# Performance work log

Measured on AMD Instinct MI355X. Metric: run time of the kernel, lower is better.

Reference implementation:

```python
import jax, jax.numpy as jnp
import numpy as np

B, S, D, H, DFF = 2, 2048, 2048, 16, 8192
DH = D // H
EPS = 1e-5


def _layer_norm(x, g, b):
    mu = jnp.mean(x, axis=-1, keepdims=True)
    var = jnp.mean(jnp.square(x - mu), axis=-1, keepdims=True)
    return (x - mu) * jax.lax.rsqrt(var + EPS) * g + b


def setup_inputs() -> dict:
    key = jax.random.key(0)
    ks = jax.random.split(key, 12)
    sc = 0.02
    inp = {
        "x": jax.random.normal(ks[0], (B, S, D), dtype=jnp.float32),
        # attention projections, stored [in, out] (torch Linear weight transposed)
        "wq": jax.random.normal(ks[1], (D, D), dtype=jnp.float32) * sc,
        "bq": jnp.zeros((D,), jnp.float32),
        "wk": jax.random.normal(ks[2], (D, D), dtype=jnp.float32) * sc,
        "bk": jnp.zeros((D,), jnp.float32),
        "wv": jax.random.normal(ks[3], (D, D), dtype=jnp.float32) * sc,
        "bv": jnp.zeros((D,), jnp.float32),
        "wo": jax.random.normal(ks[4], (D, D), dtype=jnp.float32) * sc,
        "bo": jnp.zeros((D,), jnp.float32),
        "ln1_g": jnp.ones((D,), jnp.float32),
        "ln1_b": jnp.zeros((D,), jnp.float32),
        # feed-forward
        "w1": jax.random.normal(ks[5], (D, DFF), dtype=jnp.float32) * sc,
        "b1": jnp.zeros((DFF,), jnp.float32),
        "w2": jax.random.normal(ks[6], (DFF, D), dtype=jnp.float32) * sc,
        "b2": jnp.zeros((D,), jnp.float32),
        "ln2_g": jnp.ones((D,), jnp.float32),
        "ln2_b": jnp.zeros((D,), jnp.float32),
    }
    return inp


def reference(x, wq, bq, wk, bk, wv, bv, wo, bo, ln1_g, ln1_b,
              w1, b1, w2, b2, ln2_g, ln2_b):
    # ---- MultiHeadAttentionBlock: x + MHA(LN(x)) ----
    h = _layer_norm(x, ln1_g, ln1_b)                      # [B,S,D]
    q = (h @ wq + bq).reshape(B, S, H, DH).transpose(0, 2, 1, 3)  # [B,H,S,DH]
    k = (h @ wk + bk).reshape(B, S, H, DH).transpose(0, 2, 1, 3)
    v = (h @ wv + bv).reshape(B, S, H, DH).transpose(0, 2, 1, 3)

    # faithful to source: scale by sqrt(d_dim), NOT sqrt(head_dim)
    scores = jnp.einsum("bhqd,bhkd->bhqk", q, k) / np.sqrt(D).astype(np.float32)
    # faithful triu/transpose masking (softmax sees raw zeros, not -inf)
    t = jnp.triu(scores).swapaxes(-2, -1)                 # [B,H,S,S]
    s = jax.nn.softmax(t, axis=-2)
    r = jnp.triu(s).swapaxes(-2, -1)
    attn = jnp.einsum("bhqk,bhkd->bhqd", r, v)            # [B,H,S,DH]
    attn = attn.transpose(0, 2, 1, 3).reshape(B, S, D)
    x = x + attn @ wo + bo

    # ---- FeedForwardBlock: x + FF(LN(x)), dropout rate 0 ----
    h2 = _layer_norm(x, ln2_g, ln2_b)
    ff = jax.nn.relu(h2 @ w1 + b1) @ w2 + b2
    return x + ff
```

## Files before the change

kernel.cpp:

```cpp
#include <hip/hip_runtime.h>


typedef unsigned short ushort_t;
typedef unsigned int   uint32;
typedef __attribute__((ext_vector_type(8))) short    short8;
typedef __attribute__((ext_vector_type(8))) ushort_t ushort8;
typedef __attribute__((ext_vector_type(4))) float    f32x4;

#define BDIM   2
#define SEQ    2048
#define DMODEL 2048
#define NHEAD  16
#define DHEAD  128
#define DFFN   8192
#define MROWS  (BDIM*SEQ)
#define LDQKV  6144

#define GPTR(p) (const __attribute__((address_space(1))) void*)((const void*)(p))
#define SPTR(p) (__attribute__((address_space(3))) void*)((void*)(p))

__device__ __forceinline__ float bf2f(ushort_t u) {
  union { uint32 i; float f; } c; c.i = ((uint32)u) << 16; return c.f;
}
__device__ __forceinline__ ushort_t f2bf(float f) {
  union { float f; uint32 i; } c; c.f = f;
  uint32 u = c.i;
  return (ushort_t)((u + 0x7fffu + ((u >> 16) & 1u)) >> 16);
}

__global__ __launch_bounds__(256) void transpose_f32_bf16_kern(
    const float* __restrict__ W, ushort_t* __restrict__ Wt, int K, int N)
{
  __shared__ float tile[32][33];
  const int nb = blockIdx.x * 32, kb = blockIdx.y * 32;
  const int tx = threadIdx.x & 31, ty = threadIdx.x >> 5;
#pragma unroll
  for (int j = 0; j < 32; j += 8)
    tile[ty + j][tx] = W[(size_t)(kb + ty + j) * N + nb + tx];
  __syncthreads();
#pragma unroll
  for (int j = 0; j < 32; j += 8)
    Wt[(size_t)(nb + ty + j) * K + kb + tx] = f2bf(tile[tx][ty + j]);
}

__global__ __launch_bounds__(256) void bias_concat_kern(
    const float* __restrict__ a, const float* __restrict__ b,
    const float* __restrict__ c, float* __restrict__ o)
{
  const int i = blockIdx.x * 256 + threadIdx.x;
  o[i] = (i < 2048) ? a[i] : ((i < 4096) ? b[i - 2048] : c[i - 4096]);
}

__global__ __launch_bounds__(256) void ln_kern(
    const float* __restrict__ X, const float* __restrict__ G,
    const float* __restrict__ Bb, ushort_t* __restrict__ Out)
{
  const int row = blockIdx.x, tid = threadIdx.x;
  const float* xr = X + (size_t)row * DMODEL;
  float4 v0 = ((const float4*)xr)[tid * 2];
  float4 v1 = ((const float4*)xr)[tid * 2 + 1];
  float s  = v0.x + v0.y + v0.z + v0.w + v1.x + v1.y + v1.z + v1.w;
  float ss = v0.x*v0.x + v0.y*v0.y + v0.z*v0.z + v0.w*v0.w
           + v1.x*v1.x + v1.y*v1.y + v1.z*v1.z + v1.w*v1.w;
#pragma unroll
  for (int off = 32; off > 0; off >>= 1) {
    s  += __shfl_down(s, off);
    ss += __shfl_down(ss, off);
  }
  __shared__ float rs[4], rss[4];
  __shared__ float sh_mu, sh_rst;
  const int wv = tid >> 6;
  if ((tid & 63) == 0) { rs[wv] = s; rss[wv] = ss; }
  __syncthreads();
  if (tid == 0) {
    float S1 = rs[0] + rs[1] + rs[2] + rs[3];
    float S2 = rss[0] + rss[1] + rss[2] + rss[3];
    float mu = S1 * (1.f / DMODEL);
    float var = S2 * (1.f / DMODEL) - mu * mu;
    sh_mu = mu;
    sh_rst = rsqrtf(var + 1e-5f);
  }
  __syncthreads();
  const float mu = sh_mu, rst = sh_rst;
  float4 g0 = ((const float4*)G)[tid * 2];
  float4 g1 = ((const float4*)G)[tid * 2 + 1];
  float4 b0 = ((const float4*)Bb)[tid * 2];
  float4 b1 = ((const float4*)Bb)[tid * 2 + 1];
  ushort8 o;
  o[0] = f2bf((v0.x - mu) * rst * g0.x + b0.x);
  o[1] = f2bf((v0.y - mu) * rst * g0.y + b0.y);
  o[2] = f2bf((v0.z - mu) * rst * g0.z + b0.z);
  o[3] = f2bf((v0.w - mu) * rst * g0.w + b0.w);
  o[4] = f2bf((v1.x - mu) * rst * g1.x + b1.x);
  o[5] = f2bf((v1.y - mu) * rst * g1.y + b1.y);
  o[6] = f2bf((v1.z - mu) * rst * g1.z + b1.z);
  o[7] = f2bf((v1.w - mu) * rst * g1.w + b1.w);
  *(ushort8*)(Out + (size_t)row * DMODEL + tid * 8) = o;
}

template<int OUT, int RELU, int RESID, int KDIV>
__global__ __launch_bounds__(512, 2) void gemm8_kern(
    const ushort_t* __restrict__ A, const ushort_t* __restrict__ Bt,
    const float* __restrict__ bias, const float* __restrict__ resid,
    void* __restrict__ Cout, int M, int N, int K)
{
  __shared__ ushort_t sA[4 * 8192];
  __shared__ ushort_t sB[4 * 8192];

  const int tid = threadIdx.x;
  const int nM  = gridDim.y;
  const int nwg = gridDim.x * nM;
  const int bid = blockIdx.y * gridDim.x + blockIdx.x;
  const int cpx = nwg >> 3;
  const int swz = (bid & 7) * cpx + (bid >> 3);
  const int m0 = (swz % nM) * 256;
  const int n0 = (swz / nM) * 256;

  const int Keff = K / KDIV;
  const int k0 = (KDIV > 1) ? blockIdx.z * Keff : 0;
  const int T = Keff >> 6;

  const int l = tid & 63, w = tid >> 6;
  const int lr = l & 15, lg = l >> 4;
  const int wr = w >> 2, wc = w & 3;

  const int xch   = (lg ^ ((lr >> 1) & 3)) * 8;
  const int abase = (wr * 128 + lr) * 32 + xch;
  const int bbase = (wc * 64  + lr) * 32 + xch;

  const int sr = tid >> 2;
  const int sg = ((tid & 3) ^ ((tid >> 3) & 3)) * 8;
  const ushort_t* Asrc = A  + (size_t)(m0 + sr) * K + k0 + sg;
  const ushort_t* Bsrc = Bt + (size_t)(n0 + sr) * K + k0 + sg;
  ushort_t* dA = sA + tid * 8;
  ushort_t* dB = sB + tid * 8;

#define SA_(slot, kt, kk, r) __builtin_amdgcn_global_load_lds( \
    GPTR(Asrc + (size_t)(r) * 128 * K + (kt) * 64 + (kk) * 32), \
    SPTR(dA + (slot) * 8192 + (r) * 4096), 16, 0, 0)
#define SB_(slot, kt, kk, r) __builtin_amdgcn_global_load_lds( \
    GPTR(Bsrc + (size_t)(r) * 128 * K + (kt) * 64 + (kk) * 32), \
    SPTR(dB + (slot) * 8192 + (r) * 4096), 16, 0, 0)

  f32x4 acc[8][4] = {};

  SA_(0, 0, 0, 0); SA_(0, 0, 0, 1); SB_(0, 0, 0, 0); SB_(0, 0, 0, 1);
  SA_(1, 0, 1, 0); SA_(1, 0, 1, 1); SB_(1, 0, 1, 0); SB_(1, 0, 1, 1);
  SA_(2, 1, 0, 0); SA_(2, 1, 0, 1); SB_(2, 1, 0, 0); SB_(2, 1, 0, 1);
  asm volatile("s_waitcnt vmcnt(8)" ::: "memory");
  __builtin_amdgcn_s_barrier();

  for (int t = 0; t < T; ++t) {
    const int c = t & 1;
    const ushort_t* A0 = sA + (c * 2 + 0) * 8192;
    const ushort_t* B0 = sB + (c * 2 + 0) * 8192;
    const ushort_t* A1 = sA + (c * 2 + 1) * 8192;
    const ushort_t* B1 = sB + (c * 2 + 1) * 8192;
    const int s1 = (c ^ 1) * 2 + 1;
    const int s0 = c * 2;
    const bool pf1 = (t + 1 < T), pf0 = (t + 2 < T);

    short8 a0, a1, a2, a3, b0, b1, b2, b3;

    b0 = *(const short8*)(B0 + bbase);
    b1 = *(const short8*)(B0 + bbase + 512);
    b2 = *(const short8*)(B0 + bbase + 1024);
    b3 = *(const short8*)(B0 + bbase + 1536);
    a0 = *(const short8*)(A0 + abase);
    a1 = *(const short8*)(A0 + abase + 512);
    a2 = *(const short8*)(A0 + abase + 1024);
    a3 = *(const short8*)(A0 + abase + 1536);
    if (pf1) { SA_(s1, t + 1, 1, 0); SA_(s1, t + 1, 1, 1); }
    __builtin_amdgcn_s_setprio(1);
    acc[0][0] = __builtin_amdgcn_mfma_f32_16x16x32_bf16(a0, b0, acc[0][0], 0, 0, 0);
    acc[0][1] = __builtin_amdgcn_mfma_f32_16x16x32_bf16(a0, b1, acc[0][1], 0, 0, 0);
    acc[0][2] = __builtin_amdgcn_mfma_f32_16x16x32_bf16(a0, b2, acc[0][2], 0, 0, 0);
    acc[0][3] = __builtin_amdgcn_mfma_f32_16x16x32_bf16(a0, b3, acc[0][3], 0, 0, 0);
    acc[1][0] = __builtin_amdgcn_mfma_f32_16x16x32_bf16(a1, b0, acc[1][0], 0, 0, 0);
    acc[1][1] = __builtin_amdgcn_mfma_f32_16x16x32_bf16(a1, b1, acc[1][1], 0, 0, 0);
    acc[1][2] = __builtin_amdgcn_mfma_f32_16x16x32_bf16(a1, b2, acc[1][2], 0, 0, 0);
    acc[1][3] = __builtin_amdgcn_mfma_f32_16x16x32_bf16(a1, b3, acc[1][3], 0, 0, 0);
    acc[2][0] = __builtin_amdgcn_mfma_f32_16x16x32_bf16(a2, b0, acc[2][0], 0, 0, 0);
    acc[2][1] = __builtin_amdgcn_mfma_f32_16x16x32_bf16(a2, b1, acc[2][1], 0, 0, 0);
    acc[2][2] = __builtin_amdgcn_mfma_f32_16x16x32_bf16(a2, b2, acc[2][2], 0, 0, 0);
    acc[2][3] = __builtin_amdgcn_mfma_f32_16x16x32_bf16(a2, b3, acc[2][3], 0, 0, 0);
    acc[3][0] = __builtin_amdgcn_mfma_f32_16x16x32_bf16(a3, b0, acc[3][0], 0, 0, 0);
    acc[3][1] = __builtin_amdgcn_mfma_f32_16x16x32_bf16(a3, b1, acc[3][1], 0, 0, 0);
    acc[3][2] = __builtin_amdgcn_mfma_f32_16x16x32_bf16(a3, b2, acc[3][2], 0, 0, 0);
    acc[3][3] = __builtin_amdgcn_mfma_f32_16x16x32_bf16(a3, b3, acc[3][3], 0, 0, 0);
    __builtin_amdgcn_s_setprio(0);

    a0 = *(const short8*)(A0 + abase + 2048);
    a1 = *(const short8*)(A0 + abase + 2560);
    a2 = *(const short8*)(A0 + abase + 3072);
    a3 = *(const short8*)(A0 + abase + 3584);
    if (pf1) { SB_(s1, t + 1, 1, 0); SB_(s1, t + 1, 1, 1); }
    __builtin_amdgcn_s_setprio(1);
    acc[4][0] = __builtin_amdgcn_mfma_f32_16x16x32_bf16(a0, b0, acc[4][0], 0, 0, 0);
    acc[4][1] = __builtin_amdgcn_mfma_f32_16x16x32_bf16(a0, b1, acc[4][1], 0, 0, 0);
    acc[4][2] = __builtin_amdgcn_mfma_f32_16x16x32_bf16(a0, b2, acc[4][2], 0, 0, 0);
    acc[4][3] = __builtin_amdgcn_mfma_f32_16x16x32_bf16(a0, b3, acc[4][3], 0, 0, 0);
    acc[5][0] = __builtin_amdgcn_mfma_f32_16x16x32_bf16(a1, b0, acc[5][0], 0, 0, 0);
    acc[5][1] = __builtin_amdgcn_mfma_f32_16x16x32_bf16(a1, b1, acc[5][1], 0, 0, 0);
    acc[5][2] = __builtin_amdgcn_mfma_f32_16x16x32_bf16(a1, b2, acc[5][2], 0, 0, 0);
    acc[5][3] = __builtin_amdgcn_mfma_f32_16x16x32_bf16(a1, b3, acc[5][3], 0, 0, 0);
    acc[6][0] = __builtin_amdgcn_mfma_f32_16x16x32_bf16(a2, b0, acc[6][0], 0, 0, 0);
    acc[6][1] = __builtin_amdgcn_mfma_f32_16x16x32_bf16(a2, b1, acc[6][1], 0, 0, 0);
    acc[6][2] = __builtin_amdgcn_mfma_f32_16x16x32_bf16(a2, b2, acc[6][2], 0, 0, 0);
    acc[6][3] = __builtin_amdgcn_mfma_f32_16x16x32_bf16(a2, b3, acc[6][3], 0, 0, 0);
    acc[7][0] = __builtin_amdgcn_mfma_f32_16x16x32_bf16(a3, b0, acc[7][0], 0, 0, 0);
    acc[7][1] = __builtin_amdgcn_mfma_f32_16x16x32_bf16(a3, b1, acc[7][1], 0, 0, 0);
    acc[7][2] = __builtin_amdgcn_mfma_f32_16x16x32_bf16(a3, b2, acc[7][2], 0, 0, 0);
    acc[7][3] = __builtin_amdgcn_mfma_f32_16x16x32_bf16(a3, b3, acc[7][3], 0, 0, 0);
    __builtin_amdgcn_s_setprio(0);
    if (t < T - 2) { asm volatile("s_waitcnt vmcnt(8)" ::: "memory"); }
    else           { asm volatile("s_waitcnt vmcnt(0)" ::: "memory"); }
    __builtin_amdgcn_s_barrier();

    b0 = *(const short8*)(B1 + bbase);
    b1 = *(const short8*)(B1 + bbase + 512);
    b2 = *(const short8*)(B1 + bbase + 1024);
    b3 = *(const short8*)(B1 + bbase + 1536);
    a0 = *(const short8*)(A1 + abase);
    a1 = *(const short8*)(A1 + abase + 512);
    a2 = *(const short8*)(A1 + abase + 1024);
    a3 = *(const short8*)(A1 + abase + 1536);
    if (pf0) { SA_(s0, t + 2, 0, 0); SA_(s0, t + 2, 0, 1); }
    __builtin_amdgcn_s_setprio(1);
    acc[0][0] = __builtin_amdgcn_mfma_f32_16x16x32_bf16(a0, b0, acc[0][0], 0, 0, 0);
    acc[0][1] = __builtin_amdgcn_mfma_f32_16x16x32_bf16(a0, b1, acc[0][1], 0, 0, 0);
    acc[0][2] = __builtin_amdgcn_mfma_f32_16x16x32_bf16(a0, b2, acc[0][2], 0, 0, 0);
    acc[0][3] = __builtin_amdgcn_mfma_f32_16x16x32_bf16(a0, b3, acc[0][3], 0, 0, 0);
    acc[1][0] = __builtin_amdgcn_mfma_f32_16x16x32_bf16(a1, b0, acc[1][0], 0, 0, 0);
    acc[1][1] = __builtin_amdgcn_mfma_f32_16x16x32_bf16(a1, b1, acc[1][1], 0, 0, 0);
    acc[1][2] = __builtin_amdgcn_mfma_f32_16x16x32_bf16(a1, b2, acc[1][2], 0, 0, 0);
    acc[1][3] = __builtin_amdgcn_mfma_f32_16x16x32_bf16(a1, b3, acc[1][3], 0, 0, 0);
    acc[2][0] = __builtin_amdgcn_mfma_f32_16x16x32_bf16(a2, b0, acc[2][0], 0, 0, 0);
    acc[2][1] = __builtin_amdgcn_mfma_f32_16x16x32_bf16(a2, b1, acc[2][1], 0, 0, 0);
    acc[2][2] = __builtin_amdgcn_mfma_f32_16x16x32_bf16(a2, b2, acc[2][2], 0, 0, 0);
    acc[2][3] = __builtin_amdgcn_mfma_f32_16x16x32_bf16(a2, b3, acc[2][3], 0, 0, 0);
    acc[3][0] = __builtin_amdgcn_mfma_f32_16x16x32_bf16(a3, b0, acc[3][0], 0, 0, 0);
    acc[3][1] = __builtin_amdgcn_mfma_f32_16x16x32_bf16(a3, b1, acc[3][1], 0, 0, 0);
    acc[3][2] = __builtin_amdgcn_mfma_f32_16x16x32_bf16(a3, b2, acc[3][2], 0, 0, 0);
    acc[3][3] = __builtin_amdgcn_mfma_f32_16x16x32_bf16(a3, b3, acc[3][3], 0, 0, 0);
    __builtin_amdgcn_s_setprio(0);

    a0 = *(const short8*)(A1 + abase + 2048);
    a1 = *(const short8*)(A1 + abase + 2560);
    a2 = *(const short8*)(A1 + abase + 3072);
    a3 = *(const short8*)(A1 + abase + 3584);
    if (pf0) { SB_(s0, t + 2, 0, 0); SB_(s0, t + 2, 0, 1); }
    __builtin_amdgcn_s_setprio(1);
    acc[4][0] = __builtin_amdgcn_mfma_f32_16x16x32_bf16(a0, b0, acc[4][0], 0, 0, 0);
    acc[4][1] = __builtin_amdgcn_mfma_f32_16x16x32_bf16(a0, b1, acc[4][1], 0, 0, 0);
    acc[4][2] = __builtin_amdgcn_mfma_f32_16x16x32_bf16(a0, b2, acc[4][2], 0, 0, 0);
    acc[4][3] = __builtin_amdgcn_mfma_f32_16x16x32_bf16(a0, b3, acc[4][3], 0, 0, 0);
    acc[5][0] = __builtin_amdgcn_mfma_f32_16x16x32_bf16(a1, b0, acc[5][0], 0, 0, 0);
    acc[5][1] = __builtin_amdgcn_mfma_f32_16x16x32_bf16(a1, b1, acc[5][1], 0, 0, 0);
    acc[5][2] = __builtin_amdgcn_mfma_f32_16x16x32_bf16(a1, b2, acc[5][2], 0, 0, 0);
    acc[5][3] = __builtin_amdgcn_mfma_f32_16x16x32_bf16(a1, b3, acc[5][3], 0, 0, 0);
    acc[6][0] = __builtin_amdgcn_mfma_f32_16x16x32_bf16(a2, b0, acc[6][0], 0, 0, 0);
    acc[6][1] = __builtin_amdgcn_mfma_f32_16x16x32_bf16(a2, b1, acc[6][1], 0, 0, 0);
    acc[6][2] = __builtin_amdgcn_mfma_f32_16x16x32_bf16(a2, b2, acc[6][2], 0, 0, 0);
    acc[6][3] = __builtin_amdgcn_mfma_f32_16x16x32_bf16(a2, b3, acc[6][3], 0, 0, 0);
    acc[7][0] = __builtin_amdgcn_mfma_f32_16x16x32_bf16(a3, b0, acc[7][0], 0, 0, 0);
    acc[7][1] = __builtin_amdgcn_mfma_f32_16x16x32_bf16(a3, b1, acc[7][1], 0, 0, 0);
    acc[7][2] = __builtin_amdgcn_mfma_f32_16x16x32_bf16(a3, b2, acc[7][2], 0, 0, 0);
    acc[7][3] = __builtin_amdgcn_mfma_f32_16x16x32_bf16(a3, b3, acc[7][3], 0, 0, 0);
    __builtin_amdgcn_s_setprio(0);
    if (t < T - 2) { asm volatile("s_waitcnt vmcnt(8)" ::: "memory"); }
    else           { asm volatile("s_waitcnt vmcnt(0)" ::: "memory"); }
    __builtin_amdgcn_s_barrier();
  }
#undef SA_
#undef SB_

  ushort_t* Pz = (OUT == 2)
      ? (ushort_t*)Cout + (size_t)blockIdx.z * M * N : (ushort_t*)Cout;
#pragma unroll
  for (int mi = 0; mi < 8; ++mi) {
#pragma unroll
    for (int ni = 0; ni < 4; ++ni) {
      const int gn = n0 + wc * 64 + ni * 16 + lr;
      const float bvv = (OUT == 2) ? 0.f : bias[gn];
#pragma unroll
      for (int j = 0; j < 4; ++j) {
        const int gm = m0 + wr * 128 + mi * 16 + lg * 4 + j;
        float v = acc[mi][ni][j] + bvv;
        if (RESID) v += resid[(size_t)gm * N + gn];
        if (RELU) v = fmaxf(v, 0.f);
        if (OUT == 0)      ((float*)Cout)[(size_t)gm * N + gn] = v;
        else               Pz[(size_t)gm * N + gn] = f2bf(v);
      }
    }
  }
}

__global__ __launch_bounds__(256) void combine_kern(
    const ushort_t* __restrict__ pp, const float* __restrict__ bias,
    const float* __restrict__ resid, float* __restrict__ out)
{
  const size_t i = ((size_t)blockIdx.x * 256 + threadIdx.x) * 8;
  ushort8 p0 = *(const ushort8*)(pp + i);
  ushort8 p1 = *(const ushort8*)(pp + (size_t)MROWS * 2048 + i);
  const int col = (int)(i & 2047);
  float4 r0 = *(const float4*)(resid + i);
  float4 r1 = *(const float4*)(resid + i + 4);
  float4 c0 = *(const float4*)(bias + col);
  float4 c1 = *(const float4*)(bias + col + 4);
  float4 o0, o1;
  o0.x = bf2f(p0[0]) + bf2f(p1[0]) + c0.x + r0.x;
  o0.y = bf2f(p0[1]) + bf2f(p1[1]) + c0.y + r0.y;
  o0.z = bf2f(p0[2]) + bf2f(p1[2]) + c0.z + r0.z;
  o0.w = bf2f(p0[3]) + bf2f(p1[3]) + c0.w + r0.w;
  o1.x = bf2f(p0[4]) + bf2f(p1[4]) + c1.x + r1.x;
  o1.y = bf2f(p0[5]) + bf2f(p1[5]) + c1.y + r1.y;
  o1.z = bf2f(p0[6]) + bf2f(p1[6]) + c1.z + r1.z;
  o1.w = bf2f(p0[7]) + bf2f(p1[7]) + c1.w + r1.w;
  *(float4*)(out + i) = o0;
  *(float4*)(out + i + 4) = o1;
}

__global__ __launch_bounds__(256) void attn_stats_kern(
    const ushort_t* __restrict__ Q, const ushort_t* __restrict__ Kb,
    float* __restrict__ E, float* __restrict__ DG, int ld)
{
  __shared__ ushort_t Ksm[64 * 128];
  const int qb = blockIdx.x;
  const int bh = blockIdx.y;
  const int b = bh >> 4, h = bh & 15;
  const int tid = threadIdx.x;
  const int l = tid & 63, w = tid >> 6;
  const int lr = l & 15, lg = l >> 4;

  const int qrow0 = qb * 64 + w * 16;

  const size_t qoff = (size_t)(b * SEQ + qrow0 + lr) * ld + h * DHEAD + lg * 8;
  short8 af[4];
#pragma unroll
  for (int c = 0; c < 4; ++c) af[c] = *(const short8*)(Q + qoff + c * 32);

  const int srow_b = w * 16 + (l >> 4);
  const ushort_t* Kg = Kb + (size_t)b * SEQ * ld + (size_t)h * DHEAD;
  ushort_t* Sbase = Ksm + w * 2048;

  f32x4 sume = {0.f, 0.f, 0.f, 0.f};
  f32x4 dge  = {0.f, 0.f, 0.f, 0.f};
  const float scale = 0.0220970869120796f;
  const int rx = lr & 7;

  for (int kc = qb; kc < 32; ++kc) {
    __syncthreads();
#pragma unroll
    for (int c = 0; c < 4; ++c) {
      const int row = srow_b + c * 4;
      const int g = (l & 15) ^ (row & 7);
      __builtin_amdgcn_global_load_lds(
          GPTR(Kg + (size_t)(kc * 64 + row) * ld + g * 8),
          SPTR(Sbase + c * 512), 16, 0, 0);
    }
    __syncthreads();

    const int ks0 = (kc == qb) ? w : 0;
    for (int ks = ks0; ks < 4; ++ks) {
      short8 bfr[4];
#pragma unroll
      for (int c = 0; c < 4; ++c)
        bfr[c] = *(const short8*)(Ksm + (ks * 16 + lr) * 128 + ((lg + c * 4) ^ rx) * 8);
      f32x4 sc = {0.f, 0.f, 0.f, 0.f};
      sc = __builtin_amdgcn_mfma_f32_16x16x32_bf16(af[0], bfr[0], sc, 0, 0, 0);
      sc = __builtin_amdgcn_mfma_f32_16x16x32_bf16(af[1], bfr[1], sc, 0, 0, 0);
      sc = __builtin_amdgcn_mfma_f32_16x16x32_bf16(af[2], bfr[2], sc, 0, 0, 0);
      sc = __builtin_amdgcn_mfma_f32_16x16x32_bf16(af[3], bfr[3], sc, 0, 0, 0);
      if (kc == qb && ks == w) {
        const int ki = kc * 64 + ks * 16 + lr;
#pragma unroll
        for (int j = 0; j < 4; ++j) {
          const int qi = qrow0 + lg * 4 + j;
          if (ki >= qi) {
            float e = __expf(sc[j] * scale);
            sume[j] += e;
            if (ki == qi) dge[j] += e;
          }
        }
      } else {
#pragma unroll
        for (int j = 0; j < 4; ++j)
          sume[j] += __expf(sc[j] * scale);
      }
    }
  }

#pragma unroll
  for (int j = 0; j < 4; ++j) {
#pragma unroll
    for (int off = 1; off < 16; off <<= 1) {
      sume[j] += __shfl_xor(sume[j], off);
      dge[j]  += __shfl_xor(dge[j], off);
    }
  }
  if (lr == 0) {
#pragma unroll
    for (int j = 0; j < 4; ++j) {
      E[(size_t)bh * SEQ + qrow0 + lg * 4 + j]  = sume[j];
      DG[(size_t)bh * SEQ + qrow0 + lg * 4 + j] = dge[j];
    }
  }
}

__global__ __launch_bounds__(128) void vchunk_kern(
    const ushort_t* __restrict__ V, float* __restrict__ CS, int ld)
{
  const int c = blockIdx.x, bh = blockIdx.y;
  const int b = bh >> 4, h = bh & 15;
  const int dh = threadIdx.x;
  const ushort_t* vp = V + (size_t)(b * SEQ + c * 64) * ld + h * DHEAD + dh;
  float s = 0.f;
  for (int i = 0; i < 64; ++i) s += bf2f(vp[(size_t)i * ld]);
  CS[((size_t)bh * 32 + c) * 128 + dh] = s;
}

__global__ __launch_bounds__(128) void attn_combine_kern(
    const ushort_t* __restrict__ V, const float* __restrict__ CS,
    const float* __restrict__ E, const float* __restrict__ DG,
    ushort_t* __restrict__ Attn, int ldv)
{
  const int c = blockIdx.x, bh = blockIdx.y;
  const int b = bh >> 4, h = bh & 15;
  const int dh = threadIdx.x;
  float prefix = 0.f;
  for (int cc = 0; cc < c; ++cc) prefix += CS[((size_t)bh * 32 + cc) * 128 + dh];
  const ushort_t* vp = V + (size_t)(b * SEQ + c * 64) * ldv + h * DHEAD + dh;
  ushort_t* ap = Attn + (size_t)(b * SEQ + c * 64) * DMODEL + h * DHEAD + dh;
  const int qb = c * 64;
  for (int i = 0; i < 64; ++i) {
    const int qq = qb + i;
    const float denom = (float)qq + E[(size_t)bh * SEQ + qq];
    const float de = DG[(size_t)bh * SEQ + qq];
    const float vv = bf2f(vp[(size_t)i * ldv]);
    ap[(size_t)i * DMODEL] = f2bf((prefix + de * vv) / denom);
    prefix += vv;
  }
}

extern "C" void kernel_launch(void* const* d_in, const int* in_sizes, int n_in,
                              void* d_out, int out_size, void* d_ws, size_t ws_size,
                              hipStream_t stream)
{
  const float* x    = (const float*)d_in[0];
  const float* wq   = (const float*)d_in[1];
  const float* bq   = (const float*)d_in[2];
  const float* wk   = (const float*)d_in[3];
  const float* bk   = (const float*)d_in[4];
  const float* wv   = (const float*)d_in[5];
  const float* bv   = (const float*)d_in[6];
  const float* wo   = (const float*)d_in[7];
  const float* bo   = (const float*)d_in[8];
  const float* ln1g = (const float*)d_in[9];
  const float* ln1b = (const float*)d_in[10];
  const float* w1   = (const float*)d_in[11];
  const float* b1   = (const float*)d_in[12];
  const float* w2   = (const float*)d_in[13];
  const float* b2   = (const float*)d_in[14];
  const float* ln2g = (const float*)d_in[15];
  const float* ln2b = (const float*)d_in[16];
  float* out = (float*)d_out;

  char* ws = (char*)d_ws;
  ushort_t* W1T  = (ushort_t*)(ws + 0);
  ushort_t* PPf2 = (ushort_t*)(ws + 0);
  ushort_t* W2T  = (ushort_t*)(ws + 33554432);
  ushort_t* WOT  = (ushort_t*)(ws + 67108864);
  float*    X2   = (float*)   (ws + 75497472);
  float*    Bcat = (float*)   (ws + 75497472);
  ushort_t* Hb   = (ushort_t*)(ws + 109051904);
  ushort_t* F1   = (ushort_t*)(ws + 125829120);
  ushort_t* PPwo = (ushort_t*)(ws + 125829120);
  ushort_t* WQKV = (ushort_t*)(ws + 125829120);
  ushort_t* QKVb = (ushort_t*)(ws + 150994944);
  float*    Eb   = (float*)   (ws + 201326592);
  float*    DGb  = (float*)   (ws + 201588736);
  float*    CSb  = (float*)   (ws + 201850880);

  transpose_f32_bf16_kern<<<dim3(64, 64),  256, 0, stream>>>(wq, WQKV,                   2048, 2048);
  transpose_f32_bf16_kern<<<dim3(64, 64),  256, 0, stream>>>(wk, WQKV + 2048 * 2048,     2048, 2048);
  transpose_f32_bf16_kern<<<dim3(64, 64),  256, 0, stream>>>(wv, WQKV + 2 * 2048 * 2048, 2048, 2048);
  transpose_f32_bf16_kern<<<dim3(64, 64),  256, 0, stream>>>(wo, WOT, 2048, 2048);
  transpose_f32_bf16_kern<<<dim3(256, 64), 256, 0, stream>>>(w1, W1T, 2048, 8192);
  transpose_f32_bf16_kern<<<dim3(64, 256), 256, 0, stream>>>(w2, W2T, 8192, 2048);
  bias_concat_kern<<<24, 256, 0, stream>>>(bq, bk, bv, Bcat);

  ln_kern<<<MROWS, 256, 0, stream>>>(x, ln1g, ln1b, Hb);

  gemm8_kern<1, 0, 0, 1><<<dim3(24, 16), 512, 0, stream>>>(
      Hb, WQKV, Bcat, nullptr, QKVb, MROWS, LDQKV, DMODEL);

  attn_stats_kern<<<dim3(32, 32), 256, 0, stream>>>(QKVb, QKVb + 2048, Eb, DGb, LDQKV);

  vchunk_kern<<<dim3(32, 32), 128, 0, stream>>>(QKVb + 4096, CSb, LDQKV);
  attn_combine_kern<<<dim3(32, 32), 128, 0, stream>>>(QKVb + 4096, CSb, Eb, DGb, Hb, LDQKV);

  gemm8_kern<2, 0, 0, 2><<<dim3(8, 16, 2), 512, 0, stream>>>(
      Hb, WOT, bo, nullptr, PPwo, MROWS, DMODEL, DMODEL);
  combine_kern<<<4096, 256, 0, stream>>>(PPwo, bo, x, X2);

  ln_kern<<<MROWS, 256, 0, stream>>>(X2, ln2g, ln2b, Hb);

  gemm8_kern<1, 1, 0, 1><<<dim3(32, 16), 512, 0, stream>>>(
      Hb, W1T, b1, nullptr, F1, MROWS, DFFN, DMODEL);

  gemm8_kern<2, 0, 0, 2><<<dim3(8, 16, 2), 512, 0, stream>>>(
      F1, W2T, b2, nullptr, PPf2, MROWS, DMODEL, DFFN);
  combine_kern<<<4096, 256, 0, stream>>>(PPf2, b2, X2, out);
}
```

Measured before the change: 654.2 us.

## Switch GEMMs to 32x32 MFMA, fuse weight prep and combine+LayerNorm

The GEMM kernel now uses 32x32x16 bf16 MFMA instructions with a 4x2 accumulator tile per wave instead of 16x16x32 with 8x4. This is meant to cut LDS fragment reads and instruction count per flop. Separately, the six weight transposes and the bias concat are merged into a single launch. The residual combine is fused with the second LayerNorm, removing a kernel and a pass over the activations. Risks are a changed LDS access pattern that could cause bank conflicts, and different register pressure under the 512x2 launch bounds.

```diff
diff --git a/kernel.cpp b/kernel.cpp
--- a/kernel.cpp
+++ b/kernel.cpp
@@ -3,9 +3,10 @@
 
 typedef unsigned short ushort_t;
 typedef unsigned int   uint32;
-typedef __attribute__((ext_vector_type(8))) short    short8;
-typedef __attribute__((ext_vector_type(8))) ushort_t ushort8;
-typedef __attribute__((ext_vector_type(4))) float    f32x4;
+typedef __attribute__((ext_vector_type(8)))  short    short8;
+typedef __attribute__((ext_vector_type(8)))  ushort_t ushort8;
+typedef __attribute__((ext_vector_type(4)))  float    f32x4;
+typedef __attribute__((ext_vector_type(16))) float    f32x16;
 
 #define BDIM   2
 #define SEQ    2048
@@ -28,11 +29,34 @@
   return (ushort_t)((u + 0x7fffu + ((u >> 16) & 1u)) >> 16);
 }
 
-__global__ __launch_bounds__(256) void transpose_f32_bf16_kern(
-    const float* __restrict__ W, ushort_t* __restrict__ Wt, int K, int N)
-{
+__global__ __launch_bounds__(256) void prep_kern(
+    const float* __restrict__ wq, const float* __restrict__ wk,
+    const float* __restrict__ wv, const float* __restrict__ wo,
+    const float* __restrict__ w1, const float* __restrict__ w2,
+    const float* __restrict__ bq, const float* __restrict__ bk,
+    const float* __restrict__ bv,
+    ushort_t* __restrict__ WQKV, ushort_t* __restrict__ WOT,
+    ushort_t* __restrict__ W1T, ushort_t* __restrict__ W2T,
+    float* __restrict__ Bcat)
+{
+  const int bid = blockIdx.x;
+  if (bid >= 49152) {
+    for (int i = threadIdx.x; i < 6144; i += 256)
+      Bcat[i] = (i < 2048) ? bq[i] : ((i < 4096) ? bk[i - 2048] : bv[i - 4096]);
+    return;
+  }
+  const float* W; ushort_t* Wt; int K, N, local;
+  if (bid < 12288) {
+    const int which = bid >> 12; local = bid & 4095;
+    W = (which == 0) ? wq : (which == 1) ? wk : wv;
+    Wt = WQKV + (size_t)which * 2048 * 2048; K = 2048; N = 2048;
+  } else if (bid < 16384) { W = wo; Wt = WOT; K = 2048; N = 2048; local = bid - 12288; }
+  else if (bid < 32768)   { W = w1; Wt = W1T; K = 2048; N = 8192; local = bid - 16384; }
+  else                    { W = w2; Wt = W2T; K = 8192; N = 2048; local = bid - 32768; }
+  const int ntiles = N >> 5;
+  const int nb = (local % ntiles) * 32, kb = (local / ntiles) * 32;
+
   __shared__ float tile[32][33];
-  const int nb = blockIdx.x * 32, kb = blockIdx.y * 32;
   const int tx = threadIdx.x & 31, ty = threadIdx.x >> 5;
 #pragma unroll
   for (int j = 0; j < 32; j += 8)
@@ -41,14 +65,6 @@
 #pragma unroll
   for (int j = 0; j < 32; j += 8)
     Wt[(size_t)(nb + ty + j) * K + kb + tx] = f2bf(tile[tx][ty + j]);
-}
-
-__global__ __launch_bounds__(256) void bias_concat_kern(
-    const float* __restrict__ a, const float* __restrict__ b,
-    const float* __restrict__ c, float* __restrict__ o)
-{
-  const int i = blockIdx.x * 256 + threadIdx.x;
-  o[i] = (i < 2048) ? a[i] : ((i < 4096) ? b[i - 2048] : c[i - 4096]);
 }
 
 __global__ __launch_bounds__(256) void ln_kern(
@@ -98,11 +114,58 @@
   *(ushort8*)(Out + (size_t)row * DMODEL + tid * 8) = o;
 }
 
-template<int OUT, int RELU, int RESID, int KDIV>
-__global__ __launch_bounds__(512, 2) void gemm8_kern(
+__global__ __launch_bounds__(256) void combine_ln_kern(
+    const ushort_t* __restrict__ pp, const float* __restrict__ bias,
+    const float* __restrict__ xres, const float* __restrict__ G,
+    const float* __restrict__ Bb, float* __restrict__ X2,
+    ushort_t* __restrict__ Out)
+{
+  const int row = blockIdx.x, tid = threadIdx.x;
+  const size_t i = (size_t)row * DMODEL + tid * 8;
+  ushort8 p0 = *(const ushort8*)(pp + i);
+  ushort8 p1 = *(const ushort8*)(pp + (size_t)MROWS * 2048 + i);
+  float v[8];
+#pragma unroll
+  for (int j = 0; j < 8; ++j)
+    v[j] = bf2f(p0[j]) + bf2f(p1[j]) + bias[tid * 8 + j] + xres[i + j];
+  float4 o0 = {v[0], v[1], v[2], v[3]}, o1 = {v[4], v[5], v[6], v[7]};
+  *(float4*)(X2 + i) = o0;
+  *(float4*)(X2 + i + 4) = o1;
+
+  float s = 0.f, ss = 0.f;
+#pragma unroll
+  for (int j = 0; j < 8; ++j) { s += v[j]; ss += v[j] * v[j]; }
+#pragma unroll
+  for (int off = 32; off > 0; off >>= 1) {
+    s  += __shfl_down(s, off);
+    ss += __shfl_down(ss, off);
+  }
+  __shared__ float rs[4], rss[4];
+  __shared__ float sh_mu, sh_rst;
+  const int wvv = tid >> 6;
+  if ((tid & 63) == 0) { rs[wvv] = s; rss[wvv] = ss; }
+  __syncthreads();
+  if (tid == 0) {
+    float S1 = rs[0] + rs[1] + rs[2] + rs[3];
+    float S2 = rss[0] + rss[1] + rss[2] + rss[3];
+    float mu = S1 * (1.f / DMODEL);
+    float var = S2 * (1.f / DMODEL) - mu * mu;
+    sh_mu = mu; sh_rst = rsqrtf(var + 1e-5f);
+  }
+  __syncthreads();
+  const float mu = sh_mu, rst = sh_rst;
+  ushort8 o;
+#pragma unroll
+  for (int j = 0; j < 8; ++j)
+    o[j] = f2bf((v[j] - mu) * rst * G[tid * 8 + j] + Bb[tid * 8 + j]);
+  *(ushort8*)(Out + i) = o;
+}
+
+template<int OUT, int RELU, int KDIV>
+__global__ __launch_bounds__(512, 2) void gemm32_kern(
     const ushort_t* __restrict__ A, const ushort_t* __restrict__ Bt,
-    const float* __restrict__ bias, const float* __restrict__ resid,
-    void* __restrict__ Cout, int M, int N, int K)
+    const float* __restrict__ bias, void* __restrict__ Cout,
+    int M, int N, int K)
 {
   __shared__ ushort_t sA[4 * 8192];
   __shared__ ushort_t sB[4 * 8192];
@@ -121,12 +184,14 @@
   const int T = Keff >> 6;
 
   const int l = tid & 63, w = tid >> 6;
-  const int lr = l & 15, lg = l >> 4;
+  const int l31 = l & 31, kh = l >> 5;
   const int wr = w >> 2, wc = w & 3;
 
-  const int xch   = (lg ^ ((lr >> 1) & 3)) * 8;
-  const int abase = (wr * 128 + lr) * 32 + xch;
-  const int bbase = (wc * 64  + lr) * 32 + xch;
+  const int rx2 = (l31 >> 1) & 3;
+  const int xo0 = ((0 + kh) ^ rx2) * 8;
+  const int xo1 = ((2 + kh) ^ rx2) * 8;
+  const int arow = (wr * 128 + l31) * 32;
+  const int brow = (wc * 64  + l31) * 32;
 
   const int sr = tid >> 2;
   const int sg = ((tid & 3) ^ ((tid >> 3) & 3)) * 8;
@@ -142,7 +207,7 @@
     GPTR(Bsrc + (size_t)(r) * 128 * K + (kt) * 64 + (kk) * 32), \
     SPTR(dB + (slot) * 8192 + (r) * 4096), 16, 0, 0)
 
-  f32x4 acc[8][4] = {};
+  f32x16 acc[4][2] = {};
 
   SA_(0, 0, 0, 0); SA_(0, 0, 0, 1); SB_(0, 0, 0, 0); SB_(0, 0, 0, 1);
   SA_(1, 0, 1, 0); SA_(1, 0, 1, 1); SB_(1, 0, 1, 0); SB_(1, 0, 1, 1);
@@ -151,125 +216,76 @@
   __builtin_amdgcn_s_barrier();
 
   for (int t = 0; t < T; ++t) {
-    const int c = t & 1;
-    const ushort_t* A0 = sA + (c * 2 + 0) * 8192;
-    const ushort_t* B0 = sB + (c * 2 + 0) * 8192;
-    const ushort_t* A1 = sA + (c * 2 + 1) * 8192;
-    const ushort_t* B1 = sB + (c * 2 + 1) * 8192;
-    const int s1 = (c ^ 1) * 2 + 1;
-    const int s0 = c * 2;
+    const int par = t & 1;
+    const ushort_t* pA0 = sA + (par * 2 + 0) * 8192;
+    const ushort_t* pB0 = sB + (par * 2 + 0) * 8192;
+    const ushort_t* pA1 = sA + (par * 2 + 1) * 8192;
+    const ushort_t* pB1 = sB + (par * 2 + 1) * 8192;
+    const int s1 = (par ^ 1) * 2 + 1;
+    const int s0 = par * 2;
     const bool pf1 = (t + 1 < T), pf0 = (t + 2 < T);
-
-    short8 a0, a1, a2, a3, b0, b1, b2, b3;
-
-    b0 = *(const short8*)(B0 + bbase);
-    b1 = *(const short8*)(B0 + bbase + 512);
-    b2 = *(const short8*)(B0 + bbase + 1024);
-    b3 = *(const short8*)(B0 + bbase + 1536);
-    a0 = *(const short8*)(A0 + abase);
-    a1 = *(const short8*)(A0 + abase + 512);
-    a2 = *(const short8*)(A0 + abase + 1024);
-    a3 = *(const short8*)(A0 + abase + 1536);
-    if (pf1) { SA_(s1, t + 1, 1, 0); SA_(s1, t + 1, 1, 1); }
+    const bool last2 = (t >= T - 2);
+
+    short8 aF0[4], aF1[4], bF0[2], bF1[2];
+
+#pragma unroll
+    for (int mi = 0; mi < 4; ++mi) {
+      aF0[mi] = *(const short8*)(pA0 + arow + mi * 1024 + xo0);
+      aF1[mi] = *(const short8*)(pA0 + arow + mi * 1024 + xo1);
+    }
+#pragma unroll
+    for (int ni = 0; ni < 2; ++ni) {
+      bF0[ni] = *(const short8*)(pB0 + brow + ni * 1024 + xo0);
+      bF1[ni] = *(const short8*)(pB0 + brow + ni * 1024 + xo1);
+    }
+    if (pf1) { SA_(s1, t + 1, 1, 0); SA_(s1, t + 1, 1, 1);
+               SB_(s1, t + 1, 1, 0); SB_(s1, t + 1, 1, 1); }
     __builtin_amdgcn_s_setprio(1);
-    acc[0][0] = __builtin_amdgcn_mfma_f32_16x16x32_bf16(a0, b0, acc[0][0], 0, 0, 0);
-    acc[0][1] = __builtin_amdgcn_mfma_f32_16x16x32_bf16(a0, b1, acc[0][1], 0, 0, 0);
-    acc[0][2] = __builtin_amdgcn_mfma_f32_16x16x32_bf16(a0, b2, acc[0][2], 0, 0, 0);
-    acc[0][3] = __builtin_amdgcn_mfma_f32_16x16x32_bf16(a0, b3, acc[0][3], 0, 0, 0);
-    acc[1][0] = __builtin_amdgcn_mfma_f32_16x16x32_bf16(a1, b0, acc[1][0], 0, 0, 0);
-    acc[1][1] = __builtin_amdgcn_mfma_f32_16x16x32_bf16(a1, b1, acc[1][1], 0, 0, 0);
-    acc[1][2] = __builtin_amdgcn_mfma_f32_16x16x32_bf16(a1, b2, acc[1][2], 0, 0, 0);
-    acc[1][3] = __builtin_amdgcn_mfma_f32_16x16x32_bf16(a1, b3, acc[1][3], 0, 0, 0);
-    acc[2][0] = __builtin_amdgcn_mfma_f32_16x16x32_bf16(a2, b0, acc[2][0], 0, 0, 0);
-    acc[2][1] = __builtin_amdgcn_mfma_f32_16x16x32_bf16(a2, b1, acc[2][1], 0, 0, 0);
-    acc[2][2] = __builtin_amdgcn_mfma_f32_16x16x32_bf16(a2, b2, acc[2][2], 0, 0, 0);
-    acc[2][3] = __builtin_amdgcn_mfma_f32_16x16x32_bf16(a2, b3, acc[2][3], 0, 0, 0);
-    acc[3][0] = __builtin_amdgcn_mfma_f32_16x16x32_bf16(a3, b0, acc[3][0], 0, 0, 0);
-    acc[3][1] = __builtin_amdgcn_mfma_f32_16x16x32_bf16(a3, b1, acc[3][1], 0, 0, 0);
-    acc[3][2] = __builtin_amdgcn_mfma_f32_16x16x32_bf16(a3, b2, acc[3][2], 0, 0, 0);
-    acc[3][3] = __builtin_amdgcn_mfma_f32_16x16x32_bf16(a3, b3, acc[3][3], 0, 0, 0);
+#pragma unroll
+    for (int mi = 0; mi < 4; ++mi)
+#pragma unroll
+      for (int ni = 0; ni < 2; ++ni)
+        acc[mi][ni] = __builtin_amdgcn_mfma_f32_32x32x16_bf16(
+            aF0[mi], bF0[ni], acc[mi][ni], 0, 0, 0);
+#pragma unroll
+    for (int mi = 0; mi < 4; ++mi)
+#pragma unroll
+      for (int ni = 0; ni < 2; ++ni)
+        acc[mi][ni] = __builtin_amdgcn_mfma_f32_32x32x16_bf16(
+            aF1[mi], bF1[ni], acc[mi][ni], 0, 0, 0);
     __builtin_amdgcn_s_setprio(0);
-
-    a0 = *(const short8*)(A0 + abase + 2048);
-    a1 = *(const short8*)(A0 + abase + 2560);
-    a2 = *(const short8*)(A0 + abase + 3072);
-    a3 = *(const short8*)(A0 + abase + 3584);
-    if (pf1) { SB_(s1, t + 1, 1, 0); SB_(s1, t + 1, 1, 1); }
+    if (!last2) { asm volatile("s_waitcnt vmcnt(8)" ::: "memory"); }
+    else        { asm volatile("s_waitcnt vmcnt(0)" ::: "memory"); }
+    __builtin_amdgcn_s_barrier();
+
+#pragma unroll
+    for (int mi = 0; mi < 4; ++mi) {
+      aF0[mi] = *(const short8*)(pA1 + arow + mi * 1024 + xo0);
+      aF1[mi] = *(const short8*)(pA1 + arow + mi * 1024 + xo1);
+    }
+#pragma unroll
+    for (int ni = 0; ni < 2; ++ni) {
+      bF0[ni] = *(const short8*)(pB1 + brow + ni * 1024 + xo0);
+      bF1[ni] = *(const short8*)(pB1 + brow + ni * 1024 + xo1);
+    }
+    if (pf0) { SA_(s0, t + 2, 0, 0); SA_(s0, t + 2, 0, 1);
+               SB_(s0, t + 2, 0, 0); SB_(s0, t + 2, 0, 1); }
     __builtin_amdgcn_s_setprio(1);
-    acc[4][0] = __builtin_amdgcn_mfma_f32_16x16x32_bf16(a0, b0, acc[4][0], 0, 0, 0);
-    acc[4][1] = __builtin_amdgcn_mfma_f32_16x16x32_bf16(a0, b1, acc[4][1], 0, 0, 0);
-    acc[4][2] = __builtin_amdgcn_mfma_f32_16x16x32_bf16(a0, b2, acc[4][2], 0, 0, 0);
-    acc[4][3] = __builtin_amdgcn_mfma_f32_16x16x32_bf16(a0, b3, acc[4][3], 0, 0, 0);
-    acc[5][0] = __builtin_amdgcn_mfma_f32_16x16x32_bf16(a1, b0, acc[5][0], 0, 0, 0);
-    acc[5][1] = __builtin_amdgcn_mfma_f32_16x16x32_bf16(a1, b1, acc[5][1], 0, 0, 0);
-    acc[5][2] = __builtin_amdgcn_mfma_f32_16x16x32_bf16(a1, b2, acc[5][2], 0, 0, 0);
-    acc[5][3] = __builtin_amdgcn_mfma_f32_16x16x32_bf16(a1, b3, acc[5][3], 0, 0, 0);
-    acc[6][0] = __builtin_amdgcn_mfma_f32_16x16x32_bf16(a2, b0, acc[6][0], 0, 0, 0);
-    acc[6][1] = __builtin_amdgcn_mfma_f32_16x16x32_bf16(a2, b1, acc[6][1], 0, 0, 0);
-    acc[6][2] = __builtin_amdgcn_mfma_f32_16x16x32_bf16(a2, b2, acc[6][2], 0, 0, 0);
-    acc[6][3] = __builtin_amdgcn_mfma_f32_16x16x32_bf16(a2, b3, acc[6][3], 0, 0, 0);
-    acc[7][0] = __builtin_amdgcn_mfma_f32_16x16x32_bf16(a3, b0, acc[7][0], 0, 0, 0);
-    acc[7][1] = __builtin_amdgcn_mfma_f32_16x16x32_bf16(a3, b1, acc[7][1], 0, 0, 0);
-    acc[7][2] = __builtin_amdgcn_mfma_f32_16x16x32_bf16(a3, b2, acc[7][2], 0, 0, 0);
-    acc[7][3] = __builtin_amdgcn_mfma_f32_16x16x32_bf16(a3, b3, acc[7][3], 0, 0, 0);
+#pragma unroll
+    for (int mi = 0; mi < 4; ++mi)
+#pragma unroll
+      for (int ni = 0; ni < 2; ++ni)
+        acc[mi][ni] = __builtin_amdgcn_mfma_f32_32x32x16_bf16(
+            aF0[mi], bF0[ni], acc[mi][ni], 0, 0, 0);
+#pragma unroll
+    for (int mi = 0; mi < 4; ++mi)
+#pragma unroll
+      for (int ni = 0; ni < 2; ++ni)
+        acc[mi][ni] = __builtin_amdgcn_mfma_f32_32x32x16_bf16(
+            aF1[mi], bF1[ni], acc[mi][ni], 0, 0, 0);
     __builtin_amdgcn_s_setprio(0);
-    if (t < T - 2) { asm volatile("s_waitcnt vmcnt(8)" ::: "memory"); }
-    else           { asm volatile("s_waitcnt vmcnt(0)" ::: "memory"); }
-    __builtin_amdgcn_s_barrier();
-
-    b0 = *(const short8*)(B1 + bbase);
-    b1 = *(const short8*)(B1 + bbase + 512);
-    b2 = *(const short8*)(B1 + bbase + 1024);
-    b3 = *(const short8*)(B1 + bbase + 1536);
-    a0 = *(const short8*)(A1 + abase);
-    a1 = *(const short8*)(A1 + abase + 512);
-    a2 = *(const short8*)(A1 + abase + 1024);
-    a3 = *(const short8*)(A1 + abase + 1536);
-    if (pf0) { SA_(s0, t + 2, 0, 0); SA_(s0, t + 2, 0, 1); }
-    __builtin_amdgcn_s_setprio(1);
-    acc[0][0] = __builtin_amdgcn_mfma_f32_16x16x32_bf16(a0, b0, acc[0][0], 0, 0, 0);
-    acc[0][1] = __builtin_amdgcn_mfma_f32_16x16x32_bf16(a0, b1, acc[0][1], 0, 0, 0);
-    acc[0][2] = __builtin_amdgcn_mfma_f32_16x16x32_bf16(a0, b2, acc[0][2], 0, 0, 0);
-    acc[0][3] = __builtin_amdgcn_mfma_f32_16x16x32_bf16(a0, b3, acc[0][3], 0, 0, 0);
-    acc[1][0] = __builtin_amdgcn_mfma_f32_16x16x32_bf16(a1, b0, acc[1][0], 0, 0, 0);
-    acc[1][1] = __builtin_amdgcn_mfma_f32_16x16x32_bf16(a1, b1, acc[1][1], 0, 0, 0);
-    acc[1][2] = __builtin_amdgcn_mfma_f32_16x16x32_bf16(a1, b2, acc[1][2], 0, 0, 0);
-    acc[1][3] = __builtin_amdgcn_mfma_f32_16x16x32_bf16(a1, b3, acc[1][3], 0, 0, 0);
-    acc[2][0] = __builtin_amdgcn_mfma_f32_16x16x32_bf16(a2, b0, acc[2][0], 0, 0, 0);
-    acc[2][1] = __builtin_amdgcn_mfma_f32_16x16x32_bf16(a2, b1, acc[2][1], 0, 0, 0);
-    acc[2][2] = __builtin_amdgcn_mfma_f32_16x16x32_bf16(a2, b2, acc[2][2], 0, 0, 0);
-    acc[2][3] = __builtin_amdgcn_mfma_f32_16x16x32_bf16(a2, b3, acc[2][3], 0, 0, 0);
-    acc[3][0] = __builtin_amdgcn_mfma_f32_16x16x32_bf16(a3, b0, acc[3][0], 0, 0, 0);
-    acc[3][1] = __builtin_amdgcn_mfma_f32_16x16x32_bf16(a3, b1, acc[3][1], 0, 0, 0);
-    acc[3][2] = __builtin_amdgcn_mfma_f32_16x16x32_bf16(a3, b2, acc[3][2], 0, 0, 0);
-    acc[3][3] = __builtin_amdgcn_mfma_f32_16x16x32_bf16(a3, b3, acc[3][3], 0, 0, 0);
-    __builtin_amdgcn_s_setprio(0);
-
-    a0 = *(const short8*)(A1 + abase + 2048);
-    a1 = *(const short8*)(A1 + abase + 2560);
-    a2 = *(const short8*)(A1 + abase + 3072);
-    a3 = *(const short8*)(A1 + abase + 3584);
-    if (pf0) { SB_(s0, t + 2, 0, 0); SB_(s0, t + 2, 0, 1); }
-    __builtin_amdgcn_s_setprio(1);
-    acc[4][0] = __builtin_amdgcn_mfma_f32_16x16x32_bf16(a0, b0, acc[4][0], 0, 0, 0);
-    acc[4][1] = __builtin_amdgcn_mfma_f32_16x16x32_bf16(a0, b1, acc[4][1], 0, 0, 0);
-    acc[4][2] = __builtin_amdgcn_mfma_f32_16x16x32_bf16(a0, b2, acc[4][2], 0, 0, 0);
-    acc[4][3] = __builtin_amdgcn_mfma_f32_16x16x32_bf16(a0, b3, acc[4][3], 0, 0, 0);
-    acc[5][0] = __builtin_amdgcn_mfma_f32_16x16x32_bf16(a1, b0, acc[5][0], 0, 0, 0);
-    acc[5][1] = __builtin_amdgcn_mfma_f32_16x16x32_bf16(a1, b1, acc[5][1], 0, 0, 0);
-    acc[5][2] = __builtin_amdgcn_mfma_f32_16x16x32_bf16(a1, b2, acc[5][2], 0, 0, 0);
-    acc[5][3] = __builtin_amdgcn_mfma_f32_16x16x32_bf16(a1, b3, acc[5][3], 0, 0, 0);
-    acc[6][0] = __builtin_amdgcn_mfma_f32_16x16x32_bf16(a2, b0, acc[6][0], 0, 0, 0);
-    acc[6][1] = __builtin_amdgcn_mfma_f32_16x16x32_bf16(a2, b1, acc[6][1], 0, 0, 0);
-    acc[6][2] = __builtin_amdgcn_mfma_f32_16x16x32_bf16(a2, b2, acc[6][2], 0, 0, 0);
-    acc[6][3] = __builtin_amdgcn_mfma_f32_16x16x32_bf16(a2, b3, acc[6][3], 0, 0, 0);
-    acc[7][0] = __builtin_amdgcn_mfma_f32_16x16x32_bf16(a3, b0, acc[7][0], 0, 0, 0);
-    acc[7][1] = __builtin_amdgcn_mfma_f32_16x16x32_bf16(a3, b1, acc[7][1], 0, 0, 0);
-    acc[7][2] = __builtin_amdgcn_mfma_f32_16x16x32_bf16(a3, b2, acc[7][2], 0, 0, 0);
-    acc[7][3] = __builtin_amdgcn_mfma_f32_16x16x32_bf16(a3, b3, acc[7][3], 0, 0, 0);
-    __builtin_amdgcn_s_setprio(0);
-    if (t < T - 2) { asm volatile("s_waitcnt vmcnt(8)" ::: "memory"); }
-    else           { asm volatile("s_waitcnt vmcnt(0)" ::: "memory"); }
+    if (!last2) { asm volatile("s_waitcnt vmcnt(8)" ::: "memory"); }
+    else        { asm volatile("s_waitcnt vmcnt(0)" ::: "memory"); }
     __builtin_amdgcn_s_barrier();
   }
 #undef SA_
@@ -278,19 +294,17 @@
   ushort_t* Pz = (OUT == 2)
       ? (ushort_t*)Cout + (size_t)blockIdx.z * M * N : (ushort_t*)Cout;
 #pragma unroll
-  for (int mi = 0; mi < 8; ++mi) {
-#pragma unroll
-    for (int ni = 0; ni < 4; ++ni) {
-      const int gn = n0 + wc * 64 + ni * 16 + lr;
+  for (int mi = 0; mi < 4; ++mi) {
+#pragma unroll
+    for (int ni = 0; ni < 2; ++ni) {
+      const int gn = n0 + wc * 64 + ni * 32 + l31;
       const float bvv = (OUT == 2) ? 0.f : bias[gn];
 #pragma unroll
-      for (int j = 0; j < 4; ++j) {
-        const int gm = m0 + wr * 128 + mi * 16 + lg * 4 + j;
-        float v = acc[mi][ni][j] + bvv;
-        if (RESID) v += resid[(size_t)gm * N + gn];
+      for (int reg = 0; reg < 16; ++reg) {
+        const int gm = m0 + wr * 128 + mi * 32 + (reg & 3) + 8 * (reg >> 2) + 4 * kh;
+        float v = acc[mi][ni][reg] + bvv;
         if (RELU) v = fmaxf(v, 0.f);
-        if (OUT == 0)      ((float*)Cout)[(size_t)gm * N + gn] = v;
-        else               Pz[(size_t)gm * N + gn] = f2bf(v);
+        Pz[(size_t)gm * N + gn] = f2bf(v);
       }
     }
   }
@@ -482,34 +496,28 @@
   float*    DGb  = (float*)   (ws + 201588736);
   float*    CSb  = (float*)   (ws + 201850880);
 
-  transpose_f32_bf16_kern<<<dim3(64, 64),  256, 0, stream>>>(wq, WQKV,                   2048, 2048);
-  transpose_f32_bf16_kern<<<dim3(64, 64),  256, 0, stream>>>(wk, WQKV + 2048 * 2048,     2048, 2048);
-  transpose_f32_bf16_kern<<<dim3(64, 64),  256, 0, stream>>>(wv, WQKV + 2 * 2048 * 2048, 2048, 2048);
-  transpose_f32_bf16_kern<<<dim3(64, 64),  256, 0, stream>>>(wo, WOT, 2048, 2048);
-  transpose_f32_bf16_kern<<<dim3(256, 64), 256, 0, stream>>>(w1, W1T, 2048, 8192);
-  transpose_f32_bf16_kern<<<dim3(64, 256), 256, 0, stream>>>(w2, W2T, 8192, 2048);
-  bias_concat_kern<<<24, 256, 0, stream>>>(bq, bk, bv, Bcat);
+  prep_kern<<<49153, 256, 0, stream>>>(wq, wk, wv, wo, w1, w2, bq, bk, bv,
+                                       WQKV, WOT, W1T, W2T, Bcat);
 
   ln_kern<<<MROWS, 256, 0, stream>>>(x, ln1g, ln1b, Hb);
 
-  gemm8_kern<1, 0, 0, 1><<<dim3(24, 16), 512, 0, stream>>>(
-      Hb, WQKV, Bcat, nullptr, QKVb, MROWS, LDQKV, DMODEL);
+  gemm32_kern<1, 0, 1><<<dim3(24, 16), 512, 0, stream>>>(
+      Hb, WQKV, Bcat, QKVb, MROWS, LDQKV, DMODEL);
 
   attn_stats_kern<<<dim3(32, 32), 256, 0, stream>>>(QKVb, QKVb + 2048, Eb, DGb, LDQKV);
 
   vchunk_kern<<<dim3(32, 32), 128, 0, stream>>>(QKVb + 4096, CSb, LDQKV);
   attn_combine_kern<<<dim3(32, 32), 128, 0, stream>>>(QKVb + 4096, CSb, Eb, DGb, Hb, LDQKV);
 
-  gemm8_kern<2, 0, 0, 2><<<dim3(8, 16, 2), 512, 0, stream>>>(
-      Hb, WOT, bo, nullptr, PPwo, MROWS, DMODEL, DMODEL);
-  combine_kern<<<4096, 256, 0, stream>>>(PPwo, bo, x, X2);
-
-  ln_kern<<<MROWS, 256, 0, stream>>>(X2, ln2g, ln2b, Hb);
-
-  gemm8_kern<1, 1, 0, 1><<<dim3(32, 16), 512, 0, stream>>>(
-      Hb, W1T, b1, nullptr, F1, MROWS, DFFN, DMODEL);
-
-  gemm8_kern<2, 0, 0, 2><<<dim3(8, 16, 2), 512, 0, stream>>>(
-      F1, W2T, b2, nullptr, PPf2, MROWS, DMODEL, DFFN);
+  gemm32_kern<2, 0, 2><<<dim3(8, 16, 2), 512, 0, stream>>>(
+      Hb, WOT, bo, PPwo, MROWS, DMODEL, DMODEL);
+
+  combine_ln_kern<<<MROWS, 256, 0, stream>>>(PPwo, bo, x, ln2g, ln2b, X2, Hb);
+
+  gemm32_kern<1, 1, 1><<<dim3(32, 16), 512, 0, stream>>>(
+      Hb, W1T, b1, F1, MROWS, DFFN, DMODEL);
+
+  gemm32_kern<2, 0, 2><<<dim3(8, 16, 2), 512, 0, stream>>>(
+      F1, W2T, b2, PPf2, MROWS, DMODEL, DFFN);
   combine_kern<<<4096, 256, 0, stream>>>(PPf2, b2, X2, out);
 }
```

Result: no change. 651.6 us (-0.4%).
